# Optimization experiments

Hardware: AMD Instinct MI355X
Metric: run time of the kernel (lower is better)

## Reference

```python
import jax, jax.numpy as jnp
import numpy as np

B, L1, L2, DIM_HID = 32, 64, 64, 256
FEAT = 2 * DIM_HID  # per-sequence feature dim; pair dim = 4*dim_hid


def setup_inputs() -> dict:
    key = jax.random.key(0)
    k1, k2, k3, k4, k5, k6 = jax.random.split(key, 6)
    x1 = jax.random.normal(k1, (B, L1, FEAT), dtype=jnp.float32)
    x2 = jax.random.normal(k2, (B, L2, FEAT), dtype=jnp.float32)
    # lengths in [1, L]; force max length so torch's dynamic max_len == L1*L2
    seq_lens1 = jax.random.randint(k3, (B,), 1, L1 + 1).at[0].set(L1)
    seq_lens2 = jax.random.randint(k4, (B,), 1, L2 + 1).at[0].set(L2)
    W = jax.random.normal(k5, (DIM_HID, 4 * DIM_HID), dtype=jnp.float32) * (1.0 / np.sqrt(4 * DIM_HID))
    b = jax.random.normal(k6, (DIM_HID,), dtype=jnp.float32) * 0.01
    return {"x1": x1, "seq_lens1": seq_lens1, "x2": x2, "seq_lens2": seq_lens2, "W": W, "b": b}


def reference(x1, seq_lens1, x2, seq_lens2, W, b):
    # Faithful to torch: for each sample, all (i,j) pairs with i<sl1, j<sl2 get
    # feature concat(x1[i], x2[j]); remaining rows (up to max_len = L1*L2) are
    # zero-padded BEFORE Linear+ReLU, so they contribute relu(b) to the sum.
    # Linear on concat == split GEMM: x1 @ W[:, :F].T + x2 @ W[:, F:].T + b,
    # which avoids materializing the [B, L1*L2, 4h] pair tensor.
    y1 = jnp.einsum('bif,hf->bih', x1, W[:, :FEAT])  # [B, L1, H]
    y2 = jnp.einsum('bjf,hf->bjh', x2, W[:, FEAT:])  # [B, L2, H]
    mask = (jnp.arange(L1)[None, :] < seq_lens1[:, None])[:, :, None] & \
           (jnp.arange(L2)[None, :] < seq_lens2[:, None])[:, None, :]  # [B, L1, L2]
    z = jnp.where(mask[..., None], y1[:, :, None, :] + y2[:, None, :, :] + b, b)
    y = jax.nn.relu(z)  # [B, L1, L2, H]; dropout is identity (eval / p handled)
    denom = (seq_lens1 * seq_lens2).astype(x1.dtype)[:, None]
    return y.sum(axis=(1, 2)) / denom
```

## Files before the change

kernel.cpp:

```cpp
#include <hip/hip_runtime.h>

#define BB 32
#define LL 64
#define HH 256
#define FF 512
#define WSTRIDE 1024
#define HT 32
#define BK 64
#define LSTR 72
#define YSTR 33

typedef float float4v __attribute__((ext_vector_type(4)));
typedef short short8  __attribute__((ext_vector_type(8)));

static __device__ __forceinline__ unsigned short f2bf(float x) {
    union { float f; unsigned int u; } v; v.f = x;
    v.u += 0x7FFFu + ((v.u >> 16) & 1u);
    return (unsigned short)(v.u >> 16);
}

static __device__ __forceinline__ void cvt_store16(const float4* p, unsigned short* dst) {
    const float* f = (const float*)p;
    short8 lo, hi;
    #pragma unroll
    for (int e = 0; e < 8; ++e) {
        ((unsigned short*)&lo)[e] = f2bf(f[e]);
        ((unsigned short*)&hi)[e] = f2bf(f[e + 8]);
    }
    *(short8*)dst = lo;
    *(short8*)(dst + 8) = hi;
}

static __device__ __forceinline__ void cvt_store8(const float4* p, unsigned short* dst) {
    const float* f = (const float*)p;
    short8 lo;
    #pragma unroll
    for (int e = 0; e < 8; ++e)
        ((unsigned short*)&lo)[e] = f2bf(f[e]);
    *(short8*)dst = lo;
}

__global__ __launch_bounds__(256)
void fused_kernel(const float* __restrict__ x1,
                  const int* __restrict__ s1p,
                  const float* __restrict__ x2,
                  const int* __restrict__ s2p,
                  const float* __restrict__ W,
                  const float* __restrict__ bias,
                  float* __restrict__ out) {
    const int b  = blockIdx.x;
    const int h0 = blockIdx.y * HT;

    __shared__ __align__(16) unsigned short As1[LL][LSTR];
    __shared__ __align__(16) unsigned short As2[LL][LSTR];
    __shared__ __align__(16) unsigned short Bs1[HT][LSTR];
    __shared__ __align__(16) unsigned short Bs2[HT][LSTR];
    __shared__ float y1t[LL][YSTR];
    __shared__ float y2t[LL][YSTR];
    __shared__ float partial[8][YSTR];

    const int t      = threadIdx.x;
    const int lane   = t & 63;
    const int wid    = t >> 6;
    const int srcSel = wid >> 1;
    const int mrow   = (wid & 1) * 32;
    const int lm     = lane & 15;
    const int quad   = lane >> 4;

    const int r   = t >> 2;  const int kq  = t & 3;
    const int rw  = t >> 3;  const int kq8 = t & 7;

    const float* a1p = x1 + (size_t)(b * LL + r) * FF + kq * 16;
    const float* a2p = x2 + (size_t)(b * LL + r) * FF + kq * 16;
    const float* w1p = W + (size_t)(h0 + rw) * WSTRIDE + kq8 * 8;
    const float* w2p = W + (size_t)(h0 + rw) * WSTRIDE + FF + kq8 * 8;

    float4v acc[2][2];
    #pragma unroll
    for (int i = 0; i < 2; ++i)
        #pragma unroll
        for (int j = 0; j < 2; ++j)
            acc[i][j] = (float4v){0.f, 0.f, 0.f, 0.f};

    float4 pa1[4], pa2[4], pb1[2], pb2[2];
    #pragma unroll
    for (int q = 0; q < 4; ++q) {
        pa1[q] = *(const float4*)(a1p + q * 4);
        pa2[q] = *(const float4*)(a2p + q * 4);
    }
    #pragma unroll
    for (int q = 0; q < 2; ++q) {
        pb1[q] = *(const float4*)(w1p + q * 4);
        pb2[q] = *(const float4*)(w2p + q * 4);
    }

    const unsigned short (*Ap)[LSTR] = srcSel ? As2 : As1;
    const unsigned short (*Bp)[LSTR] = srcSel ? Bs2 : Bs1;
    const unsigned short* aF0 = &Ap[mrow + lm][quad * 8];
    const unsigned short* aF1 = &Ap[mrow + 16 + lm][quad * 8];
    const unsigned short* bF0 = &Bp[lm][quad * 8];
    const unsigned short* bF1 = &Bp[16 + lm][quad * 8];

    for (int kt = 0; kt < FF / BK; ++kt) {
        cvt_store16(pa1, &As1[r][kq * 16]);
        cvt_store16(pa2, &As2[r][kq * 16]);
        cvt_store8(pb1, &Bs1[rw][kq8 * 8]);
        cvt_store8(pb2, &Bs2[rw][kq8 * 8]);
        __syncthreads();

        if (kt + 1 < FF / BK) {
            const int ko = (kt + 1) * BK;
            #pragma unroll
            for (int q = 0; q < 4; ++q) {
                pa1[q] = *(const float4*)(a1p + ko + q * 4);
                pa2[q] = *(const float4*)(a2p + ko + q * 4);
            }
            #pragma unroll
            for (int q = 0; q < 2; ++q) {
                pb1[q] = *(const float4*)(w1p + ko + q * 4);
                pb2[q] = *(const float4*)(w2p + ko + q * 4);
            }
        }

        #pragma unroll
        for (int ks = 0; ks < 2; ++ks) {
            const short8 a0 = *(const short8*)(aF0 + ks * 32);
            const short8 a1 = *(const short8*)(aF1 + ks * 32);
            const short8 b0 = *(const short8*)(bF0 + ks * 32);
            const short8 b1 = *(const short8*)(bF1 + ks * 32);
            acc[0][0] = __builtin_amdgcn_mfma_f32_16x16x32_bf16(a0, b0, acc[0][0], 0, 0, 0);
            acc[0][1] = __builtin_amdgcn_mfma_f32_16x16x32_bf16(a0, b1, acc[0][1], 0, 0, 0);
            acc[1][0] = __builtin_amdgcn_mfma_f32_16x16x32_bf16(a1, b0, acc[1][0], 0, 0, 0);
            acc[1][1] = __builtin_amdgcn_mfma_f32_16x16x32_bf16(a1, b1, acc[1][1], 0, 0, 0);
        }
        __syncthreads();
    }

    {
        float (*yt)[YSTR] = srcSel ? y2t : y1t;
        float bv[2];
        bv[0] = srcSel ? bias[h0 + lm] : 0.0f;
        bv[1] = srcSel ? bias[h0 + 16 + lm] : 0.0f;
        #pragma unroll
        for (int im = 0; im < 2; ++im)
            #pragma unroll
            for (int in = 0; in < 2; ++in)
                #pragma unroll
                for (int j = 0; j < 4; ++j)
                    yt[mrow + im * 16 + quad * 4 + j][in * 16 + lm] = acc[im][in][j] + bv[in];
    }
    __syncthreads();

    const int n1 = s1p[b];
    const int n2 = s2p[b];
    const int h  = t & 31;
    const int ic = t >> 5;

    float r1[8];
    #pragma unroll
    for (int ii = 0; ii < 8; ++ii) {
        const int i = ic * 8 + ii;
        r1[ii] = (i < n1) ? y1t[i][h] : -1e30f;
    }

    float ac[8] = {0.f, 0.f, 0.f, 0.f, 0.f, 0.f, 0.f, 0.f};
    int j = 0;
    for (; j + 2 <= n2; j += 2) {
        const float v0 = y2t[j][h];
        const float v1 = y2t[j + 1][h];
        #pragma unroll
        for (int ii = 0; ii < 8; ++ii) {
            ac[ii] += fmaxf(r1[ii] + v0, 0.f);
            ac[ii] += fmaxf(r1[ii] + v1, 0.f);
        }
    }
    if (j < n2) {
        const float v0 = y2t[j][h];
        #pragma unroll
        for (int ii = 0; ii < 8; ++ii)
            ac[ii] += fmaxf(r1[ii] + v0, 0.f);
    }
    partial[ic][h] = ((ac[0] + ac[1]) + (ac[2] + ac[3])) + ((ac[4] + ac[5]) + (ac[6] + ac[7]));
    __syncthreads();

    if (t < 32) {
        float s = 0.f;
        #pragma unroll
        for (int ic2 = 0; ic2 < 8; ++ic2)
            s += partial[ic2][t];
        const float denom = (float)(n1 * n2);
        const float pad = (float)(LL * LL) - denom;
        out[b * HH + h0 + t] = (s + pad * fmaxf(bias[h0 + t], 0.f)) / denom;
    }
}

extern "C" void kernel_launch(void* const* d_in, const int* in_sizes, int n_in,
                              void* d_out, int out_size, void* d_ws, size_t ws_size,
                              hipStream_t stream) {
    const float* x1 = (const float*)d_in[0];
    const int*   s1 = (const int*)d_in[1];
    const float* x2 = (const float*)d_in[2];
    const int*   s2 = (const int*)d_in[3];
    const float* W  = (const float*)d_in[4];
    const float* b  = (const float*)d_in[5];
    float* out = (float*)d_out;

    fused_kernel<<<dim3(BB, HH / HT), 256, 0, stream>>>(x1, s1, x2, s2, W, b, out);
}
```

Measured before the change: 78.42 us.

## Pre-convert inputs and weights to bf16 in separate kernel, double K tile

Adds a standalone conversion kernel that turns x1, x2 and W into bf16 in workspace memory. The fused GEMM kernel then loads bf16 directly and stores it to LDS without per-block conversion, with the K tile doubled to 128 and LDS reused for the output tiles. This removes the redundant fp32-to-bf16 conversion each block previously did on W and x (W was converted 32 times), and halves global load bytes in the main kernel. In exchange it adds a second launch plus a full read/write pass over all inputs.

```diff
diff --git a/kernel.cpp b/kernel.cpp
--- a/kernel.cpp
+++ b/kernel.cpp
@@ -6,9 +6,14 @@
 #define FF 512
 #define WSTRIDE 1024
 #define HT 32
-#define BK 64
-#define LSTR 72
+#define BK 128
+#define LSTR 136
 #define YSTR 33
+
+#define NX1 (BB * LL * FF)
+#define NX  (2 * NX1)
+#define NW  (HH * WSTRIDE)
+#define NTOT (NX + NW)
 
 typedef float float4v __attribute__((ext_vector_type(4)));
 typedef short short8  __attribute__((ext_vector_type(8)));
@@ -19,45 +24,46 @@
     return (unsigned short)(v.u >> 16);
 }
 
-static __device__ __forceinline__ void cvt_store16(const float4* p, unsigned short* dst) {
-    const float* f = (const float*)p;
-    short8 lo, hi;
-    #pragma unroll
-    for (int e = 0; e < 8; ++e) {
-        ((unsigned short*)&lo)[e] = f2bf(f[e]);
-        ((unsigned short*)&hi)[e] = f2bf(f[e + 8]);
-    }
-    *(short8*)dst = lo;
-    *(short8*)(dst + 8) = hi;
-}
-
-static __device__ __forceinline__ void cvt_store8(const float4* p, unsigned short* dst) {
-    const float* f = (const float*)p;
-    short8 lo;
+__global__ __launch_bounds__(256)
+void convert_kernel(const float* __restrict__ x1,
+                    const float* __restrict__ x2,
+                    const float* __restrict__ W,
+                    unsigned short* __restrict__ xb,
+                    unsigned short* __restrict__ Wb) {
+    const int idx = (blockIdx.x * 256 + threadIdx.x) * 8;
+    const float* src;
+    unsigned short* dst;
+    if (idx < NX1)      { src = x1 + idx;          dst = xb + idx; }
+    else if (idx < NX)  { src = x2 + (idx - NX1);  dst = xb + idx; }
+    else                { src = W  + (idx - NX);   dst = Wb + (idx - NX); }
+    const float4 v0 = *(const float4*)src;
+    const float4 v1 = *(const float4*)(src + 4);
+    const float f[8] = {v0.x, v0.y, v0.z, v0.w, v1.x, v1.y, v1.z, v1.w};
+    short8 o;
     #pragma unroll
     for (int e = 0; e < 8; ++e)
-        ((unsigned short*)&lo)[e] = f2bf(f[e]);
-    *(short8*)dst = lo;
+        ((unsigned short*)&o)[e] = f2bf(f[e]);
+    *(short8*)dst = o;
 }
 
 __global__ __launch_bounds__(256)
-void fused_kernel(const float* __restrict__ x1,
+void fused_kernel(const unsigned short* __restrict__ xb,
+                  const unsigned short* __restrict__ Wb,
                   const int* __restrict__ s1p,
-                  const float* __restrict__ x2,
                   const int* __restrict__ s2p,
-                  const float* __restrict__ W,
                   const float* __restrict__ bias,
                   float* __restrict__ out) {
     const int b  = blockIdx.x;
     const int h0 = blockIdx.y * HT;
 
-    __shared__ __align__(16) unsigned short As1[LL][LSTR];
-    __shared__ __align__(16) unsigned short As2[LL][LSTR];
-    __shared__ __align__(16) unsigned short Bs1[HT][LSTR];
-    __shared__ __align__(16) unsigned short Bs2[HT][LSTR];
-    __shared__ float y1t[LL][YSTR];
-    __shared__ float y2t[LL][YSTR];
-    __shared__ float partial[8][YSTR];
+    __shared__ __align__(16) unsigned char smem[52224];
+    unsigned short (*As1)[LSTR] = (unsigned short (*)[LSTR])(smem);
+    unsigned short (*As2)[LSTR] = (unsigned short (*)[LSTR])(smem + 17408);
+    unsigned short (*Bs1)[LSTR] = (unsigned short (*)[LSTR])(smem + 34816);
+    unsigned short (*Bs2)[LSTR] = (unsigned short (*)[LSTR])(smem + 43520);
+    float (*y1t)[YSTR]    = (float (*)[YSTR])(smem);
+    float (*y2t)[YSTR]    = (float (*)[YSTR])(smem + 8448);
+    float (*partial)[YSTR] = (float (*)[YSTR])(smem + 16896);
 
     const int t      = threadIdx.x;
     const int lane   = t & 63;
@@ -70,10 +76,10 @@
     const int r   = t >> 2;  const int kq  = t & 3;
     const int rw  = t >> 3;  const int kq8 = t & 7;
 
-    const float* a1p = x1 + (size_t)(b * LL + r) * FF + kq * 16;
-    const float* a2p = x2 + (size_t)(b * LL + r) * FF + kq * 16;
-    const float* w1p = W + (size_t)(h0 + rw) * WSTRIDE + kq8 * 8;
-    const float* w2p = W + (size_t)(h0 + rw) * WSTRIDE + FF + kq8 * 8;
+    const unsigned short* a1p = xb +        (size_t)(b * LL + r) * FF + kq * 32;
+    const unsigned short* a2p = xb + NX1 +  (size_t)(b * LL + r) * FF + kq * 32;
+    const unsigned short* w1p = Wb + (size_t)(h0 + rw) * WSTRIDE + kq8 * 16;
+    const unsigned short* w2p = Wb + (size_t)(h0 + rw) * WSTRIDE + FF + kq8 * 16;
 
     float4v acc[2][2];
     #pragma unroll
@@ -82,16 +88,16 @@
         for (int j = 0; j < 2; ++j)
             acc[i][j] = (float4v){0.f, 0.f, 0.f, 0.f};
 
-    float4 pa1[4], pa2[4], pb1[2], pb2[2];
+    short8 pa1[4], pa2[4], pw1[2], pw2[2];
     #pragma unroll
     for (int q = 0; q < 4; ++q) {
-        pa1[q] = *(const float4*)(a1p + q * 4);
-        pa2[q] = *(const float4*)(a2p + q * 4);
+        pa1[q] = *(const short8*)(a1p + q * 8);
+        pa2[q] = *(const short8*)(a2p + q * 8);
     }
     #pragma unroll
     for (int q = 0; q < 2; ++q) {
-        pb1[q] = *(const float4*)(w1p + q * 4);
-        pb2[q] = *(const float4*)(w2p + q * 4);
+        pw1[q] = *(const short8*)(w1p + q * 8);
+        pw2[q] = *(const short8*)(w2p + q * 8);
     }
 
     const unsigned short (*Ap)[LSTR] = srcSel ? As2 : As1;
@@ -102,28 +108,34 @@
     const unsigned short* bF1 = &Bp[16 + lm][quad * 8];
 
     for (int kt = 0; kt < FF / BK; ++kt) {
-        cvt_store16(pa1, &As1[r][kq * 16]);
-        cvt_store16(pa2, &As2[r][kq * 16]);
-        cvt_store8(pb1, &Bs1[rw][kq8 * 8]);
-        cvt_store8(pb2, &Bs2[rw][kq8 * 8]);
+        #pragma unroll
+        for (int q = 0; q < 4; ++q) {
+            *(short8*)&As1[r][kq * 32 + q * 8] = pa1[q];
+            *(short8*)&As2[r][kq * 32 + q * 8] = pa2[q];
+        }
+        #pragma unroll
+        for (int q = 0; q < 2; ++q) {
+            *(short8*)&Bs1[rw][kq8 * 16 + q * 8] = pw1[q];
+            *(short8*)&Bs2[rw][kq8 * 16 + q * 8] = pw2[q];
+        }
         __syncthreads();
 
         if (kt + 1 < FF / BK) {
             const int ko = (kt + 1) * BK;
             #pragma unroll
             for (int q = 0; q < 4; ++q) {
-                pa1[q] = *(const float4*)(a1p + ko + q * 4);
-                pa2[q] = *(const float4*)(a2p + ko + q * 4);
+                pa1[q] = *(const short8*)(a1p + ko + q * 8);
+                pa2[q] = *(const short8*)(a2p + ko + q * 8);
             }
             #pragma unroll
             for (int q = 0; q < 2; ++q) {
-                pb1[q] = *(const float4*)(w1p + ko + q * 4);
-                pb2[q] = *(const float4*)(w2p + ko + q * 4);
+                pw1[q] = *(const short8*)(w1p + ko + q * 8);
+                pw2[q] = *(const short8*)(w2p + ko + q * 8);
             }
         }
 
         #pragma unroll
-        for (int ks = 0; ks < 2; ++ks) {
+        for (int ks = 0; ks < 4; ++ks) {
             const short8 a0 = *(const short8*)(aF0 + ks * 32);
             const short8 a1 = *(const short8*)(aF1 + ks * 32);
             const short8 b0 = *(const short8*)(bF0 + ks * 32);
@@ -205,5 +217,9 @@
     const float* b  = (const float*)d_in[5];
     float* out = (float*)d_out;
 
-    fused_kernel<<<dim3(BB, HH / HT), 256, 0, stream>>>(x1, s1, x2, s2, W, b, out);
-}
+    unsigned short* xb = (unsigned short*)d_ws;
+    unsigned short* Wb = xb + NX;
+
+    convert_kernel<<<NTOT / (256 * 8), 256, 0, stream>>>(x1, x2, W, xb, Wb);
+    fused_kernel<<<dim3(BB, HH / HT), 256, 0, stream>>>(xb, Wb, s1, s2, b, out);
+}
```

Result: faster. 76.56 us (-2.4%).
